# Kernel tuning notes

Measured on AMD Instinct MI355X. Metric: run time of the kernel, lower is better.

## Reference

```python
import jax, jax.numpy as jnp
import numpy as np

N_NODES = 200000
N_EDGES = 600000
NUM_GRAPHS = 8192
IN_CH = 32
HIDDEN = [128, 256]
MLP_HIDDEN = 256
NUM_CLASSES = 10
MAX_SIZE = 40.0
BN_EPS = 1e-5


def setup_inputs() -> dict:
    key = jax.random.key(0)
    ks = jax.random.split(key, 24)
    inp = {}
    inp["x"] = jax.random.normal(ks[0], (N_NODES, IN_CH), dtype=jnp.float32)
    inp["edge_index"] = jax.random.randint(ks[1], (2, N_EDGES), 0, N_NODES, dtype=jnp.int32)
    inp["edge_type"] = jax.random.randint(ks[2], (N_EDGES,), 0, 3, dtype=jnp.int32)
    inp["batch"] = jnp.sort(jax.random.randint(ks[3], (N_NODES,), 0, NUM_GRAPHS, dtype=jnp.int32))
    prev = IN_CH
    ki = 4
    for li, h in enumerate(HIDDEN):
        inp[f"W_conv{li}"] = jax.random.normal(ks[ki], (3, prev, h), dtype=jnp.float32) * (1.0 / np.sqrt(prev)); ki += 1
        inp[f"b_conv{li}"] = jnp.zeros((3, h), dtype=jnp.float32)
        inp[f"W_id{li}"] = jax.random.normal(ks[ki], (prev, h), dtype=jnp.float32) * (1.0 / np.sqrt(prev)); ki += 1
        inp[f"b_id{li}"] = jnp.zeros((h,), dtype=jnp.float32)
        inp[f"gamma{li}"] = jnp.ones((h,), dtype=jnp.float32)
        inp[f"beta{li}"] = jnp.zeros((h,), dtype=jnp.float32)
        prev = h
    inp["W_fc1"] = jax.random.normal(ks[ki], (HIDDEN[-1] + 1, MLP_HIDDEN), dtype=jnp.float32) * (1.0 / np.sqrt(HIDDEN[-1] + 1)); ki += 1
    inp["b_fc1"] = jnp.zeros((MLP_HIDDEN,), dtype=jnp.float32)
    inp["W_fc2"] = jax.random.normal(ks[ki], (MLP_HIDDEN, NUM_CLASSES), dtype=jnp.float32) * (1.0 / np.sqrt(MLP_HIDDEN)); ki += 1
    inp["b_fc2"] = jnp.zeros((NUM_CLASSES,), dtype=jnp.float32)
    return inp


def _gcn_relation(x, W, b, src, dst, w):
    # GCNConv(normalize=True, add_self_loops=False) restricted to edges with weight w in {0,1}
    deg = jax.ops.segment_sum(w, dst, num_segments=N_NODES)          # in-degree of targets
    dinv = jnp.where(deg > 0, 1.0 / jnp.sqrt(jnp.where(deg > 0, deg, 1.0)), 0.0)
    norm = w * dinv[src] * dinv[dst]                                  # [E]
    h = x @ W                                                          # [N, H]
    agg = jax.ops.segment_sum(h[src] * norm[:, None], dst, num_segments=N_NODES)
    return agg + b


def _layer(x, W_conv, b_conv, W_id, b_id, gamma, beta, src, dst, w_rel):
    conv = jax.vmap(lambda W, b, w: _gcn_relation(x, W, b, src, dst, w))(W_conv, b_conv, w_rel)  # [3, N, H]
    out = jnp.sum(jax.nn.relu(conv), axis=0) + jax.nn.relu(x @ W_id + b_id)
    mean = jnp.mean(out, axis=0)
    var = jnp.var(out, axis=0)
    return gamma * (out - mean) / jnp.sqrt(var + BN_EPS) + beta


def reference(x, W_conv0, b_conv0, W_id0, b_id0, gamma0, beta0,
              W_conv1, b_conv1, W_id1, b_id1, gamma1, beta1,
              W_fc1, b_fc1, W_fc2, b_fc2, edge_index, edge_type, batch):
    src, dst = edge_index[0], edge_index[1]
    # one-hot relation weights [3, E]: edge_attr[:, k] == 1 masks
    w_rel = (edge_type[None, :] == jnp.arange(3)[:, None]).astype(x.dtype)
    h = _layer(x, W_conv0, b_conv0, W_id0, b_id0, gamma0, beta0, src, dst, w_rel)
    h = _layer(h, W_conv1, b_conv1, W_id1, b_id1, gamma1, beta1, src, dst, w_rel)
    # global_add_pool
    pooled = jax.ops.segment_sum(h, batch, num_segments=NUM_GRAPHS)   # [G, H]
    counts = jax.ops.segment_sum(jnp.ones((h.shape[0],), h.dtype), batch, num_segments=NUM_GRAPHS)
    pooled = jnp.concatenate([pooled, (counts / MAX_SIZE)[:, None]], axis=1)
    out = jax.nn.relu(pooled @ W_fc1 + b_fc1)
    return out @ W_fc2 + b_fc2
```

## Files before the change

kernel.cpp:

```cpp
#include <hip/hip_runtime.h>
#include <cstdint>
#include <cstddef>

#define NN 200000
#define NE 600000
#define NG 8192
#define C0 32
#define C1 128
#define C2 256
#define MLPH 256
#define NCLS 10
#define NB (3 * NN)
#define SCAN_BPB 1024
#define SCAN_NBLK ((NB + SCAN_BPB - 1) / SCAN_BPB)
#define NREP 8

typedef __attribute__((ext_vector_type(8))) short short8b;
typedef __attribute__((ext_vector_type(4))) float f32x4;

__device__ __forceinline__ void atomAddF(float* p, float v) { unsafeAtomicAdd(p, v); }

__device__ __forceinline__ float b2f(unsigned short u) {
  union { unsigned u; float f; } v; v.u = ((unsigned)u) << 16; return v.f;
}
__device__ __forceinline__ unsigned short f2b(float f) {
  union { float f; unsigned u; } v; v.f = f;
  return (unsigned short)((v.u + 0x7FFF + ((v.u >> 16) & 1)) >> 16);
}

__global__ __launch_bounds__(256) void k_fill(float* __restrict__ p, int n, float v) {
  int i = blockIdx.x * 256 + threadIdx.x;
  if (i < n) p[i] = v;
}

__global__ __launch_bounds__(256) void k_counts(const int* __restrict__ batch, float* __restrict__ counts) {
  int n = blockIdx.x * 256 + threadIdx.x;
  if (n < NN) atomAddF(&counts[batch[n]], 1.f);
}

__global__ __launch_bounds__(256) void k_hist(const int* __restrict__ dst, const int* __restrict__ et,
                                              int* __restrict__ cnt) {
  int e = blockIdx.x * 256 + threadIdx.x;
  if (e < NE) atomicAdd(&cnt[et[e] * NN + dst[e]], 1);
}

__global__ __launch_bounds__(256) void k_dinvI(const int* __restrict__ cnt, float* __restrict__ dinv) {
  int i = blockIdx.x * 256 + threadIdx.x;
  if (i < NB) { int c = cnt[i]; dinv[i] = (c > 0) ? 1.f / sqrtf((float)c) : 0.f; }
}

__global__ __launch_bounds__(256) void k_scan1(const int* __restrict__ cnt, int* __restrict__ starts,
                                               int* __restrict__ bsum) {
  __shared__ int sh[256];
  const int b0 = blockIdx.x * SCAN_BPB + threadIdx.x * 4;
  int v[4]; int tot = 0;
#pragma unroll
  for (int j = 0; j < 4; j++) {
    int b = b0 + j;
    v[j] = tot;
    tot += (b < NB) ? cnt[b] : 0;
  }
  sh[threadIdx.x] = tot;
  __syncthreads();
  for (int ofs = 1; ofs < 256; ofs <<= 1) {
    int add = (threadIdx.x >= ofs) ? sh[threadIdx.x - ofs] : 0;
    __syncthreads();
    sh[threadIdx.x] += add;
    __syncthreads();
  }
  const int excl = (threadIdx.x == 0) ? 0 : sh[threadIdx.x - 1];
#pragma unroll
  for (int j = 0; j < 4; j++) {
    int b = b0 + j;
    if (b < NB) starts[b] = excl + v[j];
  }
  if (threadIdx.x == 255) bsum[blockIdx.x] = sh[255];
}

__global__ void k_scan2(int* __restrict__ bsum) {
  if (threadIdx.x == 0) {
    int acc = 0;
    for (int i = 0; i < SCAN_NBLK; i++) { int t = bsum[i]; bsum[i] = acc; acc += t; }
  }
}

__global__ __launch_bounds__(256) void k_scan3(int* __restrict__ starts, const int* __restrict__ bsum) {
  int b = blockIdx.x * 256 + threadIdx.x;
  if (b < NB) starts[b] += bsum[b / SCAN_BPB];
}

__global__ __launch_bounds__(256) void k_place(const int* __restrict__ src, const int* __restrict__ dst,
                                               const int* __restrict__ et, int* __restrict__ starts,
                                               int* __restrict__ esrc) {
  int e = blockIdx.x * 256 + threadIdx.x;
  if (e >= NE) return;
  int b = et[e] * NN + dst[e];
  int pos = atomicAdd(&starts[b], 1);
  esrc[pos] = src[e];
}

__global__ __launch_bounds__(256) void k_prepw(const float* __restrict__ Wid, const float* __restrict__ Wc,
                                               unsigned short* __restrict__ Wtf, int CIN_, int COUT_) {
  int i = blockIdx.x * 256 + threadIdx.x;
  if (i >= 4 * CIN_ * COUT_) return;
  int j = i & 7, lq = (i >> 3) & 63, ct = (i >> 9) & 3;
  int rest = i >> 11;
  int KK = CIN_ / 32, NP = COUT_ / 64;
  int kk = rest % KK; rest /= KK;
  int p = rest % NP; int m = rest / NP;
  int ki = kk * 32 + (lq >> 4) * 4 + (j & 3) + 16 * (j >> 2);
  int c = p * 64 + ct * 16 + (lq & 15);
  float wv = (m == 0) ? Wid[(size_t)ki * COUT_ + c] : Wc[(size_t)((m - 1) * CIN_ + ki) * COUT_ + c];
  Wtf[i] = f2b(wv);
}

template <int CIN, typename TIN>
__global__ __launch_bounds__(256) void k_agg(const int* __restrict__ starts, const int* __restrict__ esrc,
                                             const float* __restrict__ dinv, const TIN* __restrict__ h,
                                             unsigned short* __restrict__ aggXb, int lo, int nloc) {
  constexpr int TPB = (CIN == 32) ? 8 : 16;
  constexpr int V = CIN / TPB;
  const int idx = blockIdx.x * 256 + threadIdx.x;
  const int bl = idx / TPB;
  const int lane = idx % TPB;
  if (bl >= 3 * nloc) return;
  const int t = bl / nloc;
  const int bin = t * NN + lo + (bl - t * nloc);
  const int s = (bin == 0) ? 0 : starts[bin - 1];
  const int e2 = starts[bin];
  float acc[V];
#pragma unroll
  for (int j = 0; j < V; j++) acc[j] = 0.f;
  for (int i = s; i < e2; i++) {
    const int sn = esrc[i];
    const float dv = dinv[(size_t)t * NN + sn];
    if (dv == 0.f) continue;
    const TIN* hp = h + (size_t)sn * CIN + lane * V;
    if constexpr (sizeof(TIN) == 2) {
      ushort4 u0 = *(const ushort4*)hp;
      ushort4 u1 = *(const ushort4*)((const unsigned short*)hp + 4);
      acc[0] = fmaf(b2f(u0.x), dv, acc[0]); acc[1] = fmaf(b2f(u0.y), dv, acc[1]);
      acc[2] = fmaf(b2f(u0.z), dv, acc[2]); acc[3] = fmaf(b2f(u0.w), dv, acc[3]);
      if constexpr (V == 8) {
        acc[4] = fmaf(b2f(u1.x), dv, acc[4]); acc[5] = fmaf(b2f(u1.y), dv, acc[5]);
        acc[6] = fmaf(b2f(u1.z), dv, acc[6]); acc[7] = fmaf(b2f(u1.w), dv, acc[7]);
      }
    } else {
      float4 v0 = *(const float4*)hp;
      acc[0] = fmaf(v0.x, dv, acc[0]); acc[1] = fmaf(v0.y, dv, acc[1]);
      acc[2] = fmaf(v0.z, dv, acc[2]); acc[3] = fmaf(v0.w, dv, acc[3]);
    }
  }
  const float dvd = dinv[bin];
  unsigned short* op = aggXb + (size_t)bl * CIN + lane * V;
  ushort4 o0;
  o0.x = f2b(acc[0] * dvd); o0.y = f2b(acc[1] * dvd);
  o0.z = f2b(acc[2] * dvd); o0.w = f2b(acc[3] * dvd);
  *(ushort4*)op = o0;
  if constexpr (V == 8) {
    ushort4 o1;
    o1.x = f2b(acc[4] * dvd); o1.y = f2b(acc[5] * dvd);
    o1.z = f2b(acc[6] * dvd); o1.w = f2b(acc[7] * dvd);
    *(ushort4*)(op + 4) = o1;
  }
}

#define SLOAD(mm)                                                                        \
  {                                                                                      \
    const short8b* g_ = (const short8b*)Wtf + (size_t)((mm) * NP + p) * PMF;             \
    _Pragma("unroll") for (int ii_ = 0; ii_ < KK; ii_++) wreg[ii_] = g_[ii_ * 256 + tid];\
  }

#define SWRITE(mm)                                                                       \
  {                                                                                      \
    short8b* d_ = wlds + ((mm) & 1) * PMF;                                               \
    _Pragma("unroll") for (int ii_ = 0; ii_ < KK; ii_++) d_[ii_ * 256 + tid] = wreg[ii_];\
  }

#define LOADA_M(A0, A1, mm)                                                              \
  {                                                                                      \
    if constexpr ((mm) > 0) {                                                            \
      const unsigned short* ar_ = aggXb + ((size_t)((mm)-1) * nloc + ln0 + rA) * CIN;    \
      _Pragma("unroll") for (int kk_ = 0; kk_ < KK; kk_++) {                             \
        A0[kk_] = *(const ushort4*)(ar_ + kk_ * 32 + lq * 4);                            \
        A1[kk_] = *(const ushort4*)(ar_ + kk_ * 32 + 16 + lq * 4);                       \
      }                                                                                  \
    } else if constexpr (INBF16) {                                                       \
      const unsigned short* xr_ = (const unsigned short*)Xv + (size_t)nA * CIN;          \
      _Pragma("unroll") for (int kk_ = 0; kk_ < KK; kk_++) {                             \
        A0[kk_] = *(const ushort4*)(xr_ + kk_ * 32 + lq * 4);                            \
        A1[kk_] = *(const ushort4*)(xr_ + kk_ * 32 + 16 + lq * 4);                       \
      }                                                                                  \
    } else {                                                                             \
      const float* xr_ = (const float*)Xv + (size_t)nA * CIN;                            \
      _Pragma("unroll") for (int kk_ = 0; kk_ < KK; kk_++) {                             \
        float4 v0_ = *(const float4*)(xr_ + kk_ * 32 + lq * 4);                          \
        float4 v1_ = *(const float4*)(xr_ + kk_ * 32 + 16 + lq * 4);                     \
        A0[kk_] = make_ushort4(f2b(v0_.x), f2b(v0_.y), f2b(v0_.z), f2b(v0_.w));          \
        A1[kk_] = make_ushort4(f2b(v1_.x), f2b(v1_.y), f2b(v1_.z), f2b(v1_.w));          \
      }                                                                                  \
    }                                                                                    \
  }

#define COMPM(A0, A1, mm)                                                                \
  {                                                                                      \
    f32x4 acc_[4];                                                                       \
    _Pragma("unroll") for (int c_ = 0; c_ < 4; c_++) acc_[c_] = (f32x4){0.f, 0.f, 0.f, 0.f}; \
    const short8b* wb_ = wlds + ((mm) & 1) * PMF;                                        \
    _Pragma("unroll") for (int kk_ = 0; kk_ < KK; kk_++) {                               \
      union { ushort4 u4[2]; short8b v; } fa_;                                           \
      fa_.u4[0] = A0[kk_]; fa_.u4[1] = A1[kk_];                                          \
      _Pragma("unroll") for (int c_ = 0; c_ < 4; c_++)                                   \
          acc_[c_] = __builtin_amdgcn_mfma_f32_16x16x32_bf16(                            \
              fa_.v, wb_[kk_ * 256 + c_ * 64 + l], acc_[c_], 0, 0, 0);                   \
    }                                                                                    \
    const float* bp_ = ((mm) == 0) ? bid : bc + (size_t)((mm)-1) * COUT;                 \
    _Pragma("unroll") for (int c_ = 0; c_ < 4; c_++) {                                   \
      float bb_ = bp_[c0 + c_ * 16 + lr];                                                \
      _Pragma("unroll") for (int j_ = 0; j_ < 4; j_++)                                   \
          run[c_][j_] += fmaxf(acc_[c_][j_] + bb_, 0.f);                                 \
    }                                                                                    \
  }

template <int CIN, int COUT, bool INBF16, bool WRITEOUT, bool DOPOOL>
__global__ __launch_bounds__(256, 3) void k_fin(
    const void* __restrict__ Xv, const unsigned short* __restrict__ aggXb,
    int lo, int nloc, int nt, const unsigned short* __restrict__ Wtf,
    const float* __restrict__ bid, const float* __restrict__ bc,
    unsigned short* __restrict__ outb, float* __restrict__ stats,
    float* __restrict__ pooled, const int* __restrict__ batch) {
  constexpr int NP = COUT / 64;
  constexpr int KK = CIN / 32;
  constexpr int PMF = KK * 256;
  constexpr int EPI = 64 * 65 * 4 + 2 * 4 * 64 * 4 + 64 * 4;
  constexpr int SMEM_BYTES = (2 * PMF * 16 > EPI) ? 2 * PMF * 16 : EPI;
  __shared__ __align__(16) char smem[SMEM_BYTES];
  short8b* wlds = (short8b*)smem;
  float (*tile)[65] = (float(*)[65])smem;
  float* sred = (float*)(smem + 64 * 65 * 4);
  int* sbatch = (int*)(smem + 64 * 65 * 4 + 2 * 4 * 64 * 4);

  const int i = blockIdx.x;
  const int xr8 = i & 7;
  const int xq = i >> 3;
  const int p = xq % NP;
  const int ti = xq / NP;
  const int tileIdx = ti * 8 + xr8;
  if (tileIdx >= nt) return;
  const int ln0 = tileIdx * 64;
  const int n0 = lo + ln0;
  const int c0 = p * 64;
  const int tid = threadIdx.x, w = tid >> 6, l = tid & 63, lr = l & 15, lq = l >> 4;
  const int rA = w * 16 + lr;
  const int nA = n0 + rA;

  f32x4 run[4];
#pragma unroll
  for (int ct = 0; ct < 4; ct++) run[ct] = (f32x4){0.f, 0.f, 0.f, 0.f};

  short8b wreg[KK];
  ushort4 a0A[KK], a1A[KK], a0B[KK], a1B[KK];

  SLOAD(0)
  LOADA_M(a0A, a1A, 0)
  SWRITE(0)
  __syncthreads();
  SLOAD(1)
  LOADA_M(a0B, a1B, 1)
  COMPM(a0A, a1A, 0)
  SWRITE(1)
  __syncthreads();
  SLOAD(2)
  LOADA_M(a0A, a1A, 2)
  COMPM(a0B, a1B, 1)
  SWRITE(2)
  __syncthreads();
  SLOAD(3)
  LOADA_M(a0B, a1B, 3)
  COMPM(a0A, a1A, 2)
  SWRITE(3)
  __syncthreads();
  COMPM(a0B, a1B, 3)
  __syncthreads();

#pragma unroll
  for (int ct = 0; ct < 4; ct++)
#pragma unroll
    for (int j = 0; j < 4; j++) tile[w * 16 + lq * 4 + j][ct * 16 + lr] = run[ct][j];
  if (DOPOOL && tid < 64) sbatch[tid] = batch[n0 + tid];
  __syncthreads();

  if (WRITEOUT) {
    const int r = tid >> 2, cg = (tid & 3) * 16;
    ushort4 o[4];
#pragma unroll
    for (int g4 = 0; g4 < 4; g4++) {
      o[g4].x = f2b(tile[r][cg + g4 * 4 + 0]);
      o[g4].y = f2b(tile[r][cg + g4 * 4 + 1]);
      o[g4].z = f2b(tile[r][cg + g4 * 4 + 2]);
      o[g4].w = f2b(tile[r][cg + g4 * 4 + 3]);
    }
    ushort4* dst4 = (ushort4*)(outb + (size_t)(n0 + r) * COUT + c0 + cg);
#pragma unroll
    for (int g4 = 0; g4 < 4; g4++) dst4[g4] = o[g4];
  }
  {
    const int col = tid & 63, rg = tid >> 6, r0 = rg * 16;
    float s = 0.f, ss = 0.f, gs = 0.f;
    int curg = DOPOOL ? sbatch[r0] : 0;
#pragma unroll
    for (int r = 0; r < 16; r++) {
      float v = tile[r0 + r][col];
      s += v; ss += v * v;
      if (DOPOOL) {
        int g = sbatch[r0 + r];
        if (g != curg) { atomAddF(&pooled[(size_t)curg * C2 + c0 + col], gs); gs = 0.f; curg = g; }
        gs += v;
      }
    }
    if (DOPOOL) atomAddF(&pooled[(size_t)curg * C2 + c0 + col], gs);
    sred[0 * 4 * 64 + rg * 64 + col] = s;
    sred[1 * 4 * 64 + rg * 64 + col] = ss;
  }
  __syncthreads();
  if (tid < 64) {
    float s4 = sred[0 + tid] + sred[64 + tid] + sred[128 + tid] + sred[192 + tid];
    float ss4 = sred[256 + tid] + sred[320 + tid] + sred[384 + tid] + sred[448 + tid];
    float* st = stats + (size_t)(tileIdx & (NREP - 1)) * 2 * COUT;
    atomAddF(&st[c0 + tid], s4);
    atomAddF(&st[COUT + c0 + tid], ss4);
  }
}

__global__ __launch_bounds__(256) void k_bnfin(const float* __restrict__ stats, const float* __restrict__ gamma,
                                               const float* __restrict__ beta, float* __restrict__ sc,
                                               float* __restrict__ sh, int COUT) {
  int c = threadIdx.x;
  if (c < COUT) {
    float su = 0.f, ssu = 0.f;
    for (int r = 0; r < NREP; r++) {
      su += stats[(size_t)r * 2 * COUT + c];
      ssu += stats[(size_t)r * 2 * COUT + COUT + c];
    }
    const float invN = 1.f / (float)NN;
    float m = su * invN;
    float v = ssu * invN - m * m;
    float s = gamma[c] / sqrtf(v + 1e-5f);
    sc[c] = s;
    sh[c] = fmaf(-m, s, beta[c]);
  }
}

__global__ __launch_bounds__(256) void k_bnfold(unsigned short* __restrict__ o, const float* __restrict__ sc,
                                                const float* __restrict__ sh) {
  size_t i8 = ((size_t)blockIdx.x * 256 + threadIdx.x) * 8;
  if (i8 >= (size_t)NN * C1) return;
  const int c = (int)(i8 & (C1 - 1));
  ushort4 a = *(ushort4*)(o + i8);
  ushort4 b = *(ushort4*)(o + i8 + 4);
  a.x = f2b(fmaf(b2f(a.x), sc[c + 0], sh[c + 0]));
  a.y = f2b(fmaf(b2f(a.y), sc[c + 1], sh[c + 1]));
  a.z = f2b(fmaf(b2f(a.z), sc[c + 2], sh[c + 2]));
  a.w = f2b(fmaf(b2f(a.w), sc[c + 3], sh[c + 3]));
  b.x = f2b(fmaf(b2f(b.x), sc[c + 4], sh[c + 4]));
  b.y = f2b(fmaf(b2f(b.y), sc[c + 5], sh[c + 5]));
  b.z = f2b(fmaf(b2f(b.z), sc[c + 6], sh[c + 6]));
  b.w = f2b(fmaf(b2f(b.w), sc[c + 7], sh[c + 7]));
  *(ushort4*)(o + i8) = a;
  *(ushort4*)(o + i8 + 4) = b;
}

__global__ __launch_bounds__(256) void k_mlp(const float* __restrict__ pooled, const float* __restrict__ counts,
                                             const float* __restrict__ sc2, const float* __restrict__ sh2,
                                             const float* __restrict__ Wf1, const float* __restrict__ bf1,
                                             const float* __restrict__ Wf2, const float* __restrict__ bf2,
                                             float* __restrict__ out) {
  __shared__ float feat[257];
  __shared__ float hid[256];
  const int g = blockIdx.x, t = threadIdx.x;
  const float cnt = counts[g];
  feat[t] = fmaf(sc2[t], pooled[(size_t)g * C2 + t], sh2[t] * cnt);
  if (t == 0) feat[256] = cnt * 0.025f;
  __syncthreads();
  float acc = bf1[t];
  for (int i = 0; i < 257; i++) acc = fmaf(feat[i], Wf1[(size_t)i * MLPH + t], acc);
  hid[t] = fmaxf(acc, 0.f);
  __syncthreads();
  if (t < NCLS) {
    float o = bf2[t];
    for (int j = 0; j < MLPH; j++) o = fmaf(hid[j], Wf2[(size_t)j * NCLS + t], o);
    out[(size_t)g * NCLS + t] = o;
  }
}

extern "C" void kernel_launch(void* const* d_in, const int* in_sizes, int n_in,
                              void* d_out, int out_size, void* d_ws, size_t ws_size,
                              hipStream_t stream) {
  const float* x = (const float*)d_in[0];
  const int* ei = (const int*)d_in[1];
  const int* et = (const int*)d_in[2];
  const int* batch = (const int*)d_in[3];
  const float* Wc0 = (const float*)d_in[4];
  const float* bc0 = (const float*)d_in[5];
  const float* Wid0 = (const float*)d_in[6];
  const float* bid0 = (const float*)d_in[7];
  const float* gm0 = (const float*)d_in[8];
  const float* bt0 = (const float*)d_in[9];
  const float* Wc1 = (const float*)d_in[10];
  const float* bc1 = (const float*)d_in[11];
  const float* Wid1 = (const float*)d_in[12];
  const float* bid1 = (const float*)d_in[13];
  const float* gm1 = (const float*)d_in[14];
  const float* bt1 = (const float*)d_in[15];
  const float* Wf1 = (const float*)d_in[16];
  const float* bf1 = (const float*)d_in[17];
  const float* Wf2 = (const float*)d_in[18];
  const float* bf2 = (const float*)d_in[19];
  const int* srcI = ei;
  const int* dstI = ei + NE;
  float* outp = (float*)d_out;

  char* ws = (char*)d_ws;
  size_t off = 0;
  auto take = [&](size_t bytes) -> char* {
    char* p = ws + off;
    off = (off + bytes + 255) & ~(size_t)255;
    return p;
  };
  float* dinv = (float*)take((size_t)NB * 4);
  int* cnt = (int*)take((size_t)NB * 4);
  int* starts = (int*)take((size_t)NB * 4);
  int* bsum = (int*)take((size_t)SCAN_NBLK * 4);
  int* esrc = (int*)take((size_t)NE * 4);
  float* stats1 = (float*)take((size_t)NREP * 2 * C1 * 4);
  float* stats2 = (float*)take((size_t)NREP * 2 * C2 * 4);
  float* sc1 = (float*)take(C1 * 4);
  float* sh1 = (float*)take(C1 * 4);
  float* sc2 = (float*)take(C2 * 4);
  float* sh2 = (float*)take(C2 * 4);
  float* counts = (float*)take((size_t)NG * 4);
  float* pooled = (float*)take((size_t)NG * C2 * 4);
  unsigned short* Wtf1 = (unsigned short*)take((size_t)4 * C0 * C1 * 2);
  unsigned short* Wtf2 = (unsigned short*)take((size_t)4 * C1 * C2 * 2);
  unsigned short* out1 = (unsigned short*)take((size_t)NN * C1 * 2);
  const size_t min_agg = (size_t)3 * 64 * C1 * 2;
  if (off + min_agg > ws_size) {
    k_fill<<<(out_size + 255) / 256, 256, 0, stream>>>(outp, out_size, 100.f);
    return;
  }
  unsigned short* aggXb = (unsigned short*)(ws + off);
  const size_t left = ws_size - off;
  long long ch1 = (long long)(left / ((size_t)3 * C0 * 2)) & ~63LL;
  long long ch2 = (long long)(left / ((size_t)3 * C1 * 2)) & ~63LL;
  if (ch1 > NN) ch1 = NN;
  if (ch2 > NN) ch2 = NN;

  dim3 blk(256);
  hipMemsetAsync(cnt, 0, (size_t)NB * 4, stream);
  hipMemsetAsync(stats1, 0, (size_t)NREP * 2 * C1 * 4, stream);
  hipMemsetAsync(stats2, 0, (size_t)NREP * 2 * C2 * 4, stream);
  hipMemsetAsync(counts, 0, (size_t)NG * 4, stream);
  hipMemsetAsync(pooled, 0, (size_t)NG * C2 * 4, stream);

  k_hist<<<(NE + 255) / 256, blk, 0, stream>>>(dstI, et, cnt);
  k_dinvI<<<(NB + 255) / 256, blk, 0, stream>>>(cnt, dinv);
  k_counts<<<(NN + 255) / 256, blk, 0, stream>>>(batch, counts);
  k_scan1<<<SCAN_NBLK, blk, 0, stream>>>(cnt, starts, bsum);
  k_scan2<<<1, 64, 0, stream>>>(bsum);
  k_scan3<<<(NB + 255) / 256, blk, 0, stream>>>(starts, bsum);
  k_place<<<(NE + 255) / 256, blk, 0, stream>>>(srcI, dstI, et, starts, esrc);

  k_prepw<<<(4 * C0 * C1 + 255) / 256, blk, 0, stream>>>(Wid0, Wc0, Wtf1, C0, C1);
  k_prepw<<<(4 * C1 * C2 + 255) / 256, blk, 0, stream>>>(Wid1, Wc1, Wtf2, C1, C2);

  for (long long lo = 0; lo < NN; lo += ch1) {
    const int nloc = (int)((NN - lo < ch1) ? (NN - lo) : ch1);
    const int nt = nloc / 64;
    const int nt8 = (nt + 7) & ~7;
    k_agg<C0, float><<<(3 * nloc * 8 + 255) / 256, blk, 0, stream>>>(starts, esrc, dinv, x, aggXb,
                                                                     (int)lo, nloc);
    k_fin<C0, C1, false, true, false><<<nt8 * (C1 / 64), blk, 0, stream>>>(
        x, aggXb, (int)lo, nloc, nt, Wtf1, bid0, bc0, out1, stats1, nullptr, nullptr);
  }
  k_bnfin<<<1, blk, 0, stream>>>(stats1, gm0, bt0, sc1, sh1, C1);
  k_bnfold<<<(int)(((size_t)NN * C1 / 8 + 255) / 256), blk, 0, stream>>>(out1, sc1, sh1);

  for (long long lo = 0; lo < NN; lo += ch2) {
    const int nloc = (int)((NN - lo < ch2) ? (NN - lo) : ch2);
    const int nt = nloc / 64;
    const int nt8 = (nt + 7) & ~7;
    k_agg<C1, unsigned short><<<(3 * nloc * 16 + 255) / 256, blk, 0, stream>>>(starts, esrc, dinv, out1,
                                                                               aggXb, (int)lo, nloc);
    k_fin<C1, C2, true, false, true><<<nt8 * (C2 / 64), blk, 0, stream>>>(
        out1, aggXb, (int)lo, nloc, nt, Wtf2, bid1, bc1, nullptr, stats2, pooled, batch);
  }
  k_bnfin<<<1, blk, 0, stream>>>(stats2, gm1, bt1, sc2, sh2, C2);

  k_mlp<<<NG, blk, 0, stream>>>(pooled, counts, sc2, sh2, Wf1, bf1, Wf2, bf2, outp);
}
```

Measured before the change: 612.2 us.

## Process two row tiles per fin block and batch MLP over 32 graphs

Each k_fin block now computes two 64-row tiles against the same staged weight slice, so each weight slice loaded into LDS is reused twice and half as many blocks are launched. A per-tile lambda runs the epilogue (store, BN stats, pooling) twice. The MLP kernel now handles 32 graphs per block, holding features transposed in shared memory so each Wf1 load is reused across 32 graphs instead of one. The costs are more registers per thread (two sets of accumulators and A fragments, plus 32 accumulators in the MLP), which may lower occupancy, and fewer blocks to fill the GPU.

```diff
diff --git a/kernel.cpp b/kernel.cpp
--- a/kernel.cpp
+++ b/kernel.cpp
@@ -14,6 +14,7 @@
 #define SCAN_BPB 1024
 #define SCAN_NBLK ((NB + SCAN_BPB - 1) / SCAN_BPB)
 #define NREP 8
+#define MGB 32
 
 typedef __attribute__((ext_vector_type(8))) short short8b;
 typedef __attribute__((ext_vector_type(4))) float f32x4;
@@ -177,22 +178,23 @@
     _Pragma("unroll") for (int ii_ = 0; ii_ < KK; ii_++) d_[ii_ * 256 + tid] = wreg[ii_];\
   }
 
-#define LOADA_M(A0, A1, mm)                                                              \
+#define LOADA_T(A0, A1, mm, TOFF)                                                        \
   {                                                                                      \
+    const int rr_ = ln0 + (TOFF) + rA;                                                   \
     if constexpr ((mm) > 0) {                                                            \
-      const unsigned short* ar_ = aggXb + ((size_t)((mm)-1) * nloc + ln0 + rA) * CIN;    \
+      const unsigned short* ar_ = aggXb + ((size_t)((mm)-1) * nloc + rr_) * CIN;         \
       _Pragma("unroll") for (int kk_ = 0; kk_ < KK; kk_++) {                             \
         A0[kk_] = *(const ushort4*)(ar_ + kk_ * 32 + lq * 4);                            \
         A1[kk_] = *(const ushort4*)(ar_ + kk_ * 32 + 16 + lq * 4);                       \
       }                                                                                  \
     } else if constexpr (INBF16) {                                                       \
-      const unsigned short* xr_ = (const unsigned short*)Xv + (size_t)nA * CIN;          \
+      const unsigned short* xr_ = (const unsigned short*)Xv + (size_t)(lo + rr_) * CIN;  \
       _Pragma("unroll") for (int kk_ = 0; kk_ < KK; kk_++) {                             \
         A0[kk_] = *(const ushort4*)(xr_ + kk_ * 32 + lq * 4);                            \
         A1[kk_] = *(const ushort4*)(xr_ + kk_ * 32 + 16 + lq * 4);                       \
       }                                                                                  \
     } else {                                                                             \
-      const float* xr_ = (const float*)Xv + (size_t)nA * CIN;                            \
+      const float* xr_ = (const float*)Xv + (size_t)(lo + rr_) * CIN;                    \
       _Pragma("unroll") for (int kk_ = 0; kk_ < KK; kk_++) {                             \
         float4 v0_ = *(const float4*)(xr_ + kk_ * 32 + lq * 4);                          \
         float4 v1_ = *(const float4*)(xr_ + kk_ * 32 + 16 + lq * 4);                     \
@@ -202,7 +204,7 @@
     }                                                                                    \
   }
 
-#define COMPM(A0, A1, mm)                                                                \
+#define COMPM_R(A0, A1, mm, RUN)                                                         \
   {                                                                                      \
     f32x4 acc_[4];                                                                       \
     _Pragma("unroll") for (int c_ = 0; c_ < 4; c_++) acc_[c_] = (f32x4){0.f, 0.f, 0.f, 0.f}; \
@@ -218,7 +220,7 @@
     _Pragma("unroll") for (int c_ = 0; c_ < 4; c_++) {                                   \
       float bb_ = bp_[c0 + c_ * 16 + lr];                                                \
       _Pragma("unroll") for (int j_ = 0; j_ < 4; j_++)                                   \
-          run[c_][j_] += fmaxf(acc_[c_][j_] + bb_, 0.f);                                 \
+          RUN[c_][j_] += fmaxf(acc_[c_][j_] + bb_, 0.f);                                 \
     }                                                                                    \
   }
 
@@ -232,7 +234,7 @@
   constexpr int NP = COUT / 64;
   constexpr int KK = CIN / 32;
   constexpr int PMF = KK * 256;
-  constexpr int EPI = 64 * 65 * 4 + 2 * 4 * 64 * 4 + 64 * 4;
+  constexpr int EPI = 64 * 65 * 4 + 2 * 4 * 64 * 4 + 128 * 4;
   constexpr int SMEM_BYTES = (2 * PMF * 16 > EPI) ? 2 * PMF * 16 : EPI;
   __shared__ __align__(16) char smem[SMEM_BYTES];
   short8b* wlds = (short8b*)smem;
@@ -244,91 +246,108 @@
   const int xr8 = i & 7;
   const int xq = i >> 3;
   const int p = xq % NP;
-  const int ti = xq / NP;
-  const int tileIdx = ti * 8 + xr8;
-  if (tileIdx >= nt) return;
-  const int ln0 = tileIdx * 64;
+  const int tpi = xq / NP;
+  const int tp = tpi * 8 + xr8;
+  const int nt2 = (nt + 1) >> 1;
+  if (tp >= nt2) return;
+  const int t0 = tp * 2;
+  const bool have2 = (t0 + 1) < nt;
+  const int ln0 = t0 * 64;
   const int n0 = lo + ln0;
   const int c0 = p * 64;
   const int tid = threadIdx.x, w = tid >> 6, l = tid & 63, lr = l & 15, lq = l >> 4;
   const int rA = w * 16 + lr;
-  const int nA = n0 + rA;
-
-  f32x4 run[4];
-#pragma unroll
-  for (int ct = 0; ct < 4; ct++) run[ct] = (f32x4){0.f, 0.f, 0.f, 0.f};
+
+  f32x4 run0[4], run1[4];
+#pragma unroll
+  for (int ct = 0; ct < 4; ct++) { run0[ct] = (f32x4){0.f, 0.f, 0.f, 0.f}; run1[ct] = run0[ct]; }
 
   short8b wreg[KK];
-  ushort4 a0A[KK], a1A[KK], a0B[KK], a1B[KK];
+  ushort4 a00[KK], a01[KK], a10[KK], a11[KK];
 
   SLOAD(0)
-  LOADA_M(a0A, a1A, 0)
+  LOADA_T(a00, a01, 0, 0)
   SWRITE(0)
   __syncthreads();
   SLOAD(1)
-  LOADA_M(a0B, a1B, 1)
-  COMPM(a0A, a1A, 0)
+  if (have2) LOADA_T(a10, a11, 0, 64)
+  COMPM_R(a00, a01, 0, run0)
+  LOADA_T(a00, a01, 1, 0)
+  if (have2) COMPM_R(a10, a11, 0, run1)
   SWRITE(1)
   __syncthreads();
   SLOAD(2)
-  LOADA_M(a0A, a1A, 2)
-  COMPM(a0B, a1B, 1)
+  if (have2) LOADA_T(a10, a11, 1, 64)
+  COMPM_R(a00, a01, 1, run0)
+  LOADA_T(a00, a01, 2, 0)
+  if (have2) COMPM_R(a10, a11, 1, run1)
   SWRITE(2)
   __syncthreads();
   SLOAD(3)
-  LOADA_M(a0B, a1B, 3)
-  COMPM(a0A, a1A, 2)
+  if (have2) LOADA_T(a10, a11, 2, 64)
+  COMPM_R(a00, a01, 2, run0)
+  LOADA_T(a00, a01, 3, 0)
+  if (have2) COMPM_R(a10, a11, 2, run1)
   SWRITE(3)
   __syncthreads();
-  COMPM(a0B, a1B, 3)
-  __syncthreads();
-
-#pragma unroll
-  for (int ct = 0; ct < 4; ct++)
-#pragma unroll
-    for (int j = 0; j < 4; j++) tile[w * 16 + lq * 4 + j][ct * 16 + lr] = run[ct][j];
-  if (DOPOOL && tid < 64) sbatch[tid] = batch[n0 + tid];
-  __syncthreads();
-
-  if (WRITEOUT) {
-    const int r = tid >> 2, cg = (tid & 3) * 16;
-    ushort4 o[4];
-#pragma unroll
-    for (int g4 = 0; g4 < 4; g4++) {
-      o[g4].x = f2b(tile[r][cg + g4 * 4 + 0]);
-      o[g4].y = f2b(tile[r][cg + g4 * 4 + 1]);
-      o[g4].z = f2b(tile[r][cg + g4 * 4 + 2]);
-      o[g4].w = f2b(tile[r][cg + g4 * 4 + 3]);
+  if (have2) LOADA_T(a10, a11, 3, 64)
+  COMPM_R(a00, a01, 3, run0)
+  if (have2) COMPM_R(a10, a11, 3, run1)
+  __syncthreads();
+
+  if (tid < 128 && (have2 || tid < 64)) sbatch[tid] = DOPOOL ? batch[n0 + tid] : 0;
+
+  auto epi = [&](f32x4 (&RUN)[4], int TOFF) {
+#pragma unroll
+    for (int ct = 0; ct < 4; ct++)
+#pragma unroll
+      for (int j = 0; j < 4; j++) tile[w * 16 + lq * 4 + j][ct * 16 + lr] = RUN[ct][j];
+    __syncthreads();
+    if (WRITEOUT) {
+      const int r = tid >> 2, cg = (tid & 3) * 16;
+      ushort4 o[4];
+#pragma unroll
+      for (int g4 = 0; g4 < 4; g4++) {
+        o[g4].x = f2b(tile[r][cg + g4 * 4 + 0]);
+        o[g4].y = f2b(tile[r][cg + g4 * 4 + 1]);
+        o[g4].z = f2b(tile[r][cg + g4 * 4 + 2]);
+        o[g4].w = f2b(tile[r][cg + g4 * 4 + 3]);
+      }
+      ushort4* dst4 = (ushort4*)(outb + (size_t)(n0 + TOFF + r) * COUT + c0 + cg);
+#pragma unroll
+      for (int g4 = 0; g4 < 4; g4++) dst4[g4] = o[g4];
     }
-    ushort4* dst4 = (ushort4*)(outb + (size_t)(n0 + r) * COUT + c0 + cg);
-#pragma unroll
-    for (int g4 = 0; g4 < 4; g4++) dst4[g4] = o[g4];
-  }
-  {
-    const int col = tid & 63, rg = tid >> 6, r0 = rg * 16;
-    float s = 0.f, ss = 0.f, gs = 0.f;
-    int curg = DOPOOL ? sbatch[r0] : 0;
-#pragma unroll
-    for (int r = 0; r < 16; r++) {
-      float v = tile[r0 + r][col];
-      s += v; ss += v * v;
-      if (DOPOOL) {
-        int g = sbatch[r0 + r];
-        if (g != curg) { atomAddF(&pooled[(size_t)curg * C2 + c0 + col], gs); gs = 0.f; curg = g; }
-        gs += v;
+    {
+      const int col = tid & 63, rg = tid >> 6, r0 = rg * 16;
+      float s = 0.f, ss = 0.f, gs = 0.f;
+      int curg = DOPOOL ? sbatch[TOFF + r0] : 0;
+#pragma unroll
+      for (int r = 0; r < 16; r++) {
+        float v = tile[r0 + r][col];
+        s += v; ss += v * v;
+        if (DOPOOL) {
+          int g = sbatch[TOFF + r0 + r];
+          if (g != curg) { atomAddF(&pooled[(size_t)curg * C2 + c0 + col], gs); gs = 0.f; curg = g; }
+          gs += v;
+        }
       }
+      if (DOPOOL) atomAddF(&pooled[(size_t)curg * C2 + c0 + col], gs);
+      sred[0 * 4 * 64 + rg * 64 + col] = s;
+      sred[1 * 4 * 64 + rg * 64 + col] = ss;
     }
-    if (DOPOOL) atomAddF(&pooled[(size_t)curg * C2 + c0 + col], gs);
-    sred[0 * 4 * 64 + rg * 64 + col] = s;
-    sred[1 * 4 * 64 + rg * 64 + col] = ss;
-  }
-  __syncthreads();
-  if (tid < 64) {
-    float s4 = sred[0 + tid] + sred[64 + tid] + sred[128 + tid] + sred[192 + tid];
-    float ss4 = sred[256 + tid] + sred[320 + tid] + sred[384 + tid] + sred[448 + tid];
-    float* st = stats + (size_t)(tileIdx & (NREP - 1)) * 2 * COUT;
-    atomAddF(&st[c0 + tid], s4);
-    atomAddF(&st[COUT + c0 + tid], ss4);
+    __syncthreads();
+    if (tid < 64) {
+      float s4 = sred[0 + tid] + sred[64 + tid] + sred[128 + tid] + sred[192 + tid];
+      float ss4 = sred[256 + tid] + sred[320 + tid] + sred[384 + tid] + sred[448 + tid];
+      float* st = stats + (size_t)(t0 & (NREP - 1)) * 2 * COUT;
+      atomAddF(&st[c0 + tid], s4);
+      atomAddF(&st[COUT + c0 + tid], ss4);
+    }
+  };
+  epi(run0, 0);
+  if (have2) {
+    __syncthreads();
+    epi(run1, 64);
   }
 }
 
@@ -375,21 +394,45 @@
                                              const float* __restrict__ Wf1, const float* __restrict__ bf1,
                                              const float* __restrict__ Wf2, const float* __restrict__ bf2,
                                              float* __restrict__ out) {
-  __shared__ float feat[257];
-  __shared__ float hid[256];
-  const int g = blockIdx.x, t = threadIdx.x;
-  const float cnt = counts[g];
-  feat[t] = fmaf(sc2[t], pooled[(size_t)g * C2 + t], sh2[t] * cnt);
-  if (t == 0) feat[256] = cnt * 0.025f;
-  __syncthreads();
-  float acc = bf1[t];
-  for (int i = 0; i < 257; i++) acc = fmaf(feat[i], Wf1[(size_t)i * MLPH + t], acc);
-  hid[t] = fmaxf(acc, 0.f);
-  __syncthreads();
-  if (t < NCLS) {
-    float o = bf2[t];
-    for (int j = 0; j < MLPH; j++) o = fmaf(hid[j], Wf2[(size_t)j * NCLS + t], o);
-    out[(size_t)g * NCLS + t] = o;
+  __shared__ float featT[257 * 36];
+  __shared__ float cnts[MGB];
+  const int g0 = blockIdx.x * MGB;
+  const int t = threadIdx.x;
+  if (t < MGB) cnts[t] = counts[g0 + t];
+  __syncthreads();
+  {
+    const float sc = sc2[t], sh = sh2[t];
+    for (int g = 0; g < MGB; g++)
+      featT[t * 36 + g] = fmaf(sc, pooled[(size_t)(g0 + g) * C2 + t], sh * cnts[g]);
+  }
+  if (t < MGB) featT[256 * 36 + t] = cnts[t] * 0.025f;
+  __syncthreads();
+  float acc[MGB];
+  const float b1 = bf1[t];
+#pragma unroll
+  for (int g = 0; g < MGB; g++) acc[g] = b1;
+  for (int i = 0; i < 257; i++) {
+    const float wv = Wf1[(size_t)i * MLPH + t];
+    const float* fr = &featT[i * 36];
+#pragma unroll
+    for (int g4 = 0; g4 < MGB / 4; g4++) {
+      float4 fg = *(const float4*)(fr + g4 * 4);
+      acc[g4 * 4 + 0] = fmaf(fg.x, wv, acc[g4 * 4 + 0]);
+      acc[g4 * 4 + 1] = fmaf(fg.y, wv, acc[g4 * 4 + 1]);
+      acc[g4 * 4 + 2] = fmaf(fg.z, wv, acc[g4 * 4 + 2]);
+      acc[g4 * 4 + 3] = fmaf(fg.w, wv, acc[g4 * 4 + 3]);
+    }
+  }
+  __syncthreads();
+  float* hidT = featT;
+#pragma unroll
+  for (int g = 0; g < MGB; g++) hidT[t * 36 + g] = fmaxf(acc[g], 0.f);
+  __syncthreads();
+  for (int task = t; task < MGB * NCLS; task += 256) {
+    const int g = task / NCLS, c = task % NCLS;
+    float o = bf2[c];
+    for (int j = 0; j < MLPH; j++) o = fmaf(hidT[j * 36 + g], Wf2[(size_t)j * NCLS + c], o);
+    out[(size_t)(g0 + g) * NCLS + c] = o;
   }
 }
 
@@ -476,10 +519,11 @@
   for (long long lo = 0; lo < NN; lo += ch1) {
     const int nloc = (int)((NN - lo < ch1) ? (NN - lo) : ch1);
     const int nt = nloc / 64;
-    const int nt8 = (nt + 7) & ~7;
+    const int nt2 = (nt + 1) >> 1;
+    const int nt2_8 = (nt2 + 7) & ~7;
     k_agg<C0, float><<<(3 * nloc * 8 + 255) / 256, blk, 0, stream>>>(starts, esrc, dinv, x, aggXb,
                                                                      (int)lo, nloc);
-    k_fin<C0, C1, false, true, false><<<nt8 * (C1 / 64), blk, 0, stream>>>(
+    k_fin<C0, C1, false, true, false><<<nt2_8 * (C1 / 64), blk, 0, stream>>>(
         x, aggXb, (int)lo, nloc, nt, Wtf1, bid0, bc0, out1, stats1, nullptr, nullptr);
   }
   k_bnfin<<<1, blk, 0, stream>>>(stats1, gm0, bt0, sc1, sh1, C1);
@@ -488,13 +532,14 @@
   for (long long lo = 0; lo < NN; lo += ch2) {
     const int nloc = (int)((NN - lo < ch2) ? (NN - lo) : ch2);
     const int nt = nloc / 64;
-    const int nt8 = (nt + 7) & ~7;
+    const int nt2 = (nt + 1) >> 1;
+    const int nt2_8 = (nt2 + 7) & ~7;
     k_agg<C1, unsigned short><<<(3 * nloc * 16 + 255) / 256, blk, 0, stream>>>(starts, esrc, dinv, out1,
                                                                                aggXb, (int)lo, nloc);
-    k_fin<C1, C2, true, false, true><<<nt8 * (C2 / 64), blk, 0, stream>>>(
+    k_fin<C1, C2, true, false, true><<<nt2_8 * (C2 / 64), blk, 0, stream>>>(
         out1, aggXb, (int)lo, nloc, nt, Wtf2, bid1, bc1, nullptr, stats2, pooled, batch);
   }
   k_bnfin<<<1, blk, 0, stream>>>(stats2, gm1, bt1, sc2, sh2, C2);
 
-  k_mlp<<<NG, blk, 0, stream>>>(pooled, counts, sc2, sh2, Wf1, bf1, Wf2, bf2, outp);
-}
+  k_mlp<<<NG / MGB, blk, 0, stream>>>(pooled, counts, sc2, sh2, Wf1, bf1, Wf2, bf2, outp);
+}
```

Measured after the change: 689.4 us. 12.6% more time.
